# Optimization experiments

Hardware: AMD Instinct MI355X
Metric: run time of the kernel (lower is better)

## Reference

```python
import jax, jax.numpy as jnp
import numpy as np

N, E, IN, TD, H, C0, C1 = 50000, 800000, 128, 64, 4, 64, 16
SLOPE = 0.2


def setup_inputs() -> dict:
    key = jax.random.key(0)
    ks = jax.random.split(key, 20)
    def rn(k, shape, scale=1.0):
        return jax.random.normal(k, shape, dtype=jnp.float32) * scale
    return {
        "x": rn(ks[0], (N, IN)),
        "edge_index": jax.random.randint(ks[1], (2, E), 0, N),
        "timestamps": jax.random.uniform(ks[2], (E,), dtype=jnp.float32),
        # TimeEncoder: linear(1 -> TD) then cos, then abs
        "time_w": rn(ks[3], (TD,)),
        "time_b": rn(ks[4], (TD,)),
        # GATConv layer 0: in=IN, out-per-head=C0, heads=H
        "W0": rn(ks[5], (IN, H * C0), 0.1),
        "att_src0": rn(ks[6], (H, C0), 0.1),
        "att_dst0": rn(ks[7], (H, C0), 0.1),
        "lin_edge0": rn(ks[8], (TD, H * C0), 0.1),
        "att_edge0": rn(ks[9], (H, C0), 0.1),
        "bias0": rn(ks[10], (H * C0,), 0.1),
        # GATConv layer 1: in=H*C0, out-per-head=C1, heads=H
        "W1": rn(ks[11], (H * C0, H * C1), 0.1),
        "att_src1": rn(ks[12], (H, C1), 0.1),
        "att_dst1": rn(ks[13], (H, C1), 0.1),
        "lin_edge1": rn(ks[14], (TD, H * C1), 0.1),
        "att_edge1": rn(ks[15], (H, C1), 0.1),
        "bias1": rn(ks[16], (H * C1,), 0.1),
    }


def gat_layer(h_in, src, dst, edge_attr, W, a_src, a_dst, W_e, a_e, bias):
    """One PyG-style GATConv with edge-attr attention (concat heads, no dropout)."""
    heads = a_src.shape[0]
    HC = W.shape[1]
    C = HC // heads
    n_nodes = h_in.shape[0]
    h = (h_in @ W).reshape(n_nodes, heads, C)                 # [N, H, C]
    e = (edge_attr @ W_e).reshape(-1, heads, C)               # [Et, H, C]
    # attention logits per edge, per head
    alpha = ((h * a_src).sum(-1)[src]
             + (h * a_dst).sum(-1)[dst]
             + (e * a_e).sum(-1))                              # [Et, H]
    alpha = jnp.where(alpha >= 0, alpha, SLOPE * alpha)       # leaky relu
    # segment softmax over destination node
    m = jax.ops.segment_max(alpha, dst, num_segments=n_nodes)  # [N, H]
    ea = jnp.exp(alpha - m[dst])
    s = jax.ops.segment_sum(ea, dst, num_segments=n_nodes)
    a = ea / (s[dst] + 1e-16)                                 # [Et, H]
    # weighted scatter-add aggregation
    out = jax.ops.segment_sum(h[src] * a[..., None], dst, num_segments=n_nodes)
    return out.reshape(n_nodes, HC) + bias


def reference(x, edge_index, timestamps, time_w, time_b,
              W0, att_src0, att_dst0, lin_edge0, att_edge0, bias0,
              W1, att_src1, att_dst1, lin_edge1, att_edge1, bias1):
    # TimeEncoder -> abs, per-edge feature [E, TD]
    ef = jnp.abs(jnp.cos(timestamps[:, None] * time_w + time_b))
    # add self loops with edge_attr fill value 1.0
    loops = jnp.arange(N)
    src = jnp.concatenate([edge_index[0], loops])
    dst = jnp.concatenate([edge_index[1], loops])
    ef = jnp.concatenate([ef, jnp.ones((N, TD), ef.dtype)], axis=0)
    h = gat_layer(x, src, dst, ef, W0, att_src0, att_dst0, lin_edge0, att_edge0, bias0)
    h = gat_layer(h, src, dst, ef, W1, att_src1, att_dst1, lin_edge1, att_edge1, bias1)
    return h  # [N, H*C1] = [50000, 64]
```

## Files before the change

### kernel.cpp

```cpp
#include <hip/hip_runtime.h>
#include <math.h>

#define N_NODES 50000
#define N_EDGES 800000
#define ET (N_EDGES + N_NODES)
#define IN_F 128
#define TDIM 64
#define HEADS 4
#define C0 64
#define C1 16
#define HC0 256
#define HC1 64
#define KF 512
#define SLOPE 0.2f
#define TAB 4096
#define BSHIFT 8
#define NBUCKET 196
#define CHUNK 2048

using short8 = __attribute__((ext_vector_type(8))) short;
using f32x4 = __attribute__((ext_vector_type(4))) float;

__device__ __forceinline__ float bf2f(unsigned u16) { return __uint_as_float(u16 << 16); }
__device__ __forceinline__ unsigned short f2bf(float f) {
    unsigned u = __float_as_uint(f);
    return (unsigned short)((u + 0x7fffu + ((u >> 16) & 1u)) >> 16);
}
__device__ __forceinline__ unsigned pk2(float lo, float hi) {
    return (unsigned)f2bf(lo) | ((unsigned)f2bf(hi) << 16);
}
__device__ __forceinline__ float lrelu(float a) { return a >= 0.f ? a : SLOPE * a; }

__global__ __launch_bounds__(256) void k_param(
    const float* __restrict__ le0, const float* __restrict__ at0, const float* __restrict__ le1,
    const float* __restrict__ at1, const float* __restrict__ W0, const float* __restrict__ asr,
    const float* __restrict__ ads, const float* __restrict__ W1, const float* __restrict__ bias0,
    float* __restrict__ v0, float* __restrict__ v1, float* __restrict__ l0,
    float* __restrict__ l1, float* __restrict__ as0, float* __restrict__ ad0,
    unsigned short* __restrict__ W01t, float* __restrict__ b01) {
    int b = blockIdx.x, tid = threadIdx.x;
    int h = tid >> 6, c = tid & 63;
    if (b < 64) {
        int td = b;
        float p0 = le0[td * HC0 + h * C0 + c] * at0[h * C0 + c];
        for (int m = 1; m < 64; m <<= 1) p0 += __shfl_xor(p0, m);
        if (c == 0) v0[td * 4 + h] = p0;
        float p1 = 0.f;
        if (c < C1) p1 = le1[td * HC1 + h * C1 + c] * at1[h * C1 + c];
        for (int m = 1; m < 16; m <<= 1) p1 += __shfl_xor(p1, m);
        if (c == 0) v1[td * 4 + h] = p1;
    } else if (b == 64) {
        float s0 = 0.f;
        for (int td = 0; td < TDIM; ++td) s0 += le0[td * HC0 + h * C0 + c];
        s0 *= at0[h * C0 + c];
        for (int m = 1; m < 64; m <<= 1) s0 += __shfl_xor(s0, m);
        if (c == 0) l0[h] = s0;
        float s1 = 0.f;
        if (c < C1) {
            for (int td = 0; td < TDIM; ++td) s1 += le1[td * HC1 + h * C1 + c];
            s1 *= at1[h * C1 + c];
        }
        for (int m = 1; m < 16; m <<= 1) s1 += __shfl_xor(s1, m);
        if (c == 0) l1[h] = s1;
    } else if (b < 193) {
        int k = b - 65;
        float wv = W0[k * HC0 + h * C0 + c];
        float ps = wv * asr[h * C0 + c];
        float pd = wv * ads[h * C0 + c];
        for (int m = 1; m < 64; m <<= 1) {
            ps += __shfl_xor(ps, m);
            pd += __shfl_xor(pd, m);
        }
        if (c == 0) {
            as0[h * IN_F + k] = ps;
            ad0[h * IN_F + k] = pd;
        }
    } else if (b < 321) {
        int hk = (b - 193) * 4 + (tid >> 6);
        int c1 = tid & 63;
        int hh = hk >> 7, k = hk & 127;
        float acc = 0.f;
        for (int c0 = 0; c0 < C0; ++c0)
            acc += W0[k * HC0 + hh * C0 + c0] * W1[(size_t)(hh * C0 + c0) * HC1 + c1];
        W01t[(size_t)c1 * KF + hk] = f2bf(acc);
    } else {
        if (tid < 64) {
            float acc = 0.f;
            for (int k = 0; k < HC0; ++k) acc += bias0[k] * W1[(size_t)k * HC1 + tid];
            b01[tid] = acc;
        }
    }
}

__global__ __launch_bounds__(256) void k_aetab(const float* __restrict__ tw,
                                               const float* __restrict__ tb,
                                               const float* __restrict__ v0,
                                               const float* __restrict__ v1,
                                               float* __restrict__ tab0,
                                               float* __restrict__ tab1) {
    __shared__ float sw[TDIM], sb[TDIM], sv0[TDIM * 4], sv1[TDIM * 4];
    int tid = threadIdx.x;
    if (tid < TDIM) {
        sw[tid] = tw[tid];
        sb[tid] = tb[tid];
    }
    sv0[tid] = v0[tid];
    sv1[tid] = v1[tid];
    __syncthreads();
    int i = blockIdx.x * 256 + tid;
    if (i > TAB) return;
    float time = (float)i / (float)TAB;
    float a00 = 0, a01 = 0, a02 = 0, a03 = 0, a10 = 0, a11 = 0, a12 = 0, a13 = 0;
#pragma unroll 8
    for (int d = 0; d < TDIM; ++d) {
        float f = fabsf(__cosf(time * sw[d] + sb[d]));
        a00 += f * sv0[d * 4 + 0];
        a01 += f * sv0[d * 4 + 1];
        a02 += f * sv0[d * 4 + 2];
        a03 += f * sv0[d * 4 + 3];
        a10 += f * sv1[d * 4 + 0];
        a11 += f * sv1[d * 4 + 1];
        a12 += f * sv1[d * 4 + 2];
        a13 += f * sv1[d * 4 + 3];
    }
    ((float4*)tab0)[i] = make_float4(a00, a01, a02, a03);
    ((float4*)tab1)[i] = make_float4(a10, a11, a12, a13);
}

__global__ __launch_bounds__(256) void k_xbs(const float* __restrict__ x,
                                             const float* __restrict__ as0,
                                             const float* __restrict__ ad0,
                                             unsigned short* __restrict__ xb,
                                             float* __restrict__ ssrc, float* __restrict__ sdst) {
    int w = threadIdx.x >> 6, l = threadIdx.x & 63;
    int n = blockIdx.x * 4 + w;
    if (n >= N_NODES) return;
    float2 xv = *(const float2*)(x + (size_t)n * IN_F + l * 2);
    *(unsigned*)(xb + (size_t)n * IN_F + l * 2) = pk2(xv.x, xv.y);
    float ps[4], pd[4];
#pragma unroll
    for (int h = 0; h < 4; ++h) {
        float2 a = *(const float2*)(as0 + h * IN_F + l * 2);
        float2 d = *(const float2*)(ad0 + h * IN_F + l * 2);
        ps[h] = xv.x * a.x + xv.y * a.y;
        pd[h] = xv.x * d.x + xv.y * d.y;
    }
#pragma unroll
    for (int m = 1; m < 64; m <<= 1) {
#pragma unroll
        for (int h = 0; h < 4; ++h) {
            ps[h] += __shfl_xor(ps[h], m);
            pd[h] += __shfl_xor(pd[h], m);
        }
    }
    if (l == 0) {
#pragma unroll
        for (int h = 0; h < 4; ++h) {
            ssrc[n * 4 + h] = ps[h];
            sdst[n * 4 + h] = pd[h];
        }
    }
}

__global__ void k_count(const int* __restrict__ ei, int* __restrict__ deg) {
    int t = blockIdx.x * blockDim.x + threadIdx.x;
    if (t >= N_EDGES) return;
    atomicAdd(&deg[ei[N_EDGES + t]], 1);
}

__global__ void k_scan_block(const int* __restrict__ deg, int* __restrict__ rowptr,
                             int* __restrict__ blocksum, int n) {
    __shared__ int buf[256];
    int tid = threadIdx.x, i = blockIdx.x * 256 + tid;
    int v = (i < n) ? (deg[i] + 1) : 0;
    buf[tid] = v;
    __syncthreads();
    for (int off = 1; off < 256; off <<= 1) {
        int t = (tid >= off) ? buf[tid - off] : 0;
        __syncthreads();
        buf[tid] += t;
        __syncthreads();
    }
    if (i < n) rowptr[i + 1] = buf[tid];
    if (tid == 255) blocksum[blockIdx.x] = buf[255];
}

__global__ void k_scan_top(const int* __restrict__ blocksum, int* __restrict__ blockoff, int nb) {
    __shared__ int buf[256];
    int tid = threadIdx.x;
    int v = (tid < nb) ? blocksum[tid] : 0;
    buf[tid] = v;
    __syncthreads();
    for (int off = 1; off < 256; off <<= 1) {
        int t = (tid >= off) ? buf[tid - off] : 0;
        __syncthreads();
        buf[tid] += t;
        __syncthreads();
    }
    if (tid < nb) blockoff[tid] = buf[tid] - v;
}

__global__ void k_finalize(int* __restrict__ rowptr, const int* __restrict__ blockoff,
                           const int* __restrict__ deg, int* __restrict__ cursor,
                           int* __restrict__ edst, int* __restrict__ eord,
                           int* __restrict__ bcur) {
    int i = blockIdx.x * 256 + threadIdx.x;
    if (i >= N_NODES) return;
    int v = rowptr[i + 1] + blockoff[blockIdx.x];
    rowptr[i + 1] = v;
    int start = v - deg[i] - 1;
    cursor[i] = start;
    if (i == 0) rowptr[0] = 0;
    if ((i & 255) == 0) bcur[i >> BSHIFT] = start;
    for (int p = start; p < v; ++p) edst[p] = i;
    eord[v - 1] = N_EDGES + i;
}

__global__ __launch_bounds__(256) void k_bucketA(const int* __restrict__ ei,
                                                 int* __restrict__ bcur,
                                                 int2* __restrict__ staging) {
    __shared__ int cnt[NBUCKET], base[NBUCKET];
    int tid = threadIdx.x;
    int e0 = blockIdx.x * CHUNK;
    for (int i = tid; i < NBUCKET; i += 256) cnt[i] = 0;
    __syncthreads();
    int t[8], d[8];
#pragma unroll
    for (int i = 0; i < 8; ++i) {
        int tt = e0 + i * 256 + tid;
        t[i] = tt;
        d[i] = (tt < N_EDGES) ? ei[N_EDGES + tt] : -1;
        if (d[i] >= 0) atomicAdd(&cnt[d[i] >> BSHIFT], 1);
    }
    __syncthreads();
    for (int i = tid; i < NBUCKET; i += 256) {
        int c = cnt[i];
        base[i] = c ? atomicAdd(&bcur[i], c) : 0;
        cnt[i] = 0;
    }
    __syncthreads();
#pragma unroll
    for (int i = 0; i < 8; ++i) {
        if (d[i] >= 0) {
            int b = d[i] >> BSHIFT;
            int off = atomicAdd(&cnt[b], 1);
            staging[base[b] + off] = make_int2(t[i], d[i]);
        }
    }
}

__global__ __launch_bounds__(256) void k_bucketB(const int* __restrict__ rowptr,
                                                 const int* __restrict__ bcur,
                                                 const int2* __restrict__ staging,
                                                 int* __restrict__ cursor,
                                                 int* __restrict__ eord) {
    int b = blockIdx.x;
    int lo = rowptr[b << BSHIFT];
    int hi = bcur[b];
    for (int p = lo + threadIdx.x; p < hi; p += 256) {
        int2 td = staging[p];
        int q = atomicAdd(&cursor[td.y], 1);
        eord[q] = td.x;
    }
}

__global__ void k_expand(const int* __restrict__ eord, const int* __restrict__ ei,
                         const float* __restrict__ ts, const int* __restrict__ edst,
                         const float* __restrict__ tab0, const float* __restrict__ l0,
                         const float* __restrict__ ssrc0, const float* __restrict__ sdst0,
                         int* __restrict__ esrc, float* __restrict__ ew0p) {
    int p = blockIdx.x * blockDim.x + threadIdx.x;
    if (p >= ET) return;
    int t = eord[p], d = edst[p];
    int s;
    float4 a0;
    if (t >= N_EDGES) {
        s = t - N_EDGES;
        a0 = ((const float4*)l0)[0];
    } else {
        s = ei[t];
        float f = ts[t] * (float)TAB;
        int i = (int)f;
        i = i > TAB - 1 ? TAB - 1 : i;
        float fr = f - (float)i;
        float4 t0 = ((const float4*)tab0)[i];
        float4 t1 = ((const float4*)tab0)[i + 1];
        a0.x = t0.x + fr * (t1.x - t0.x);
        a0.y = t0.y + fr * (t1.y - t0.y);
        a0.z = t0.z + fr * (t1.z - t0.z);
        a0.w = t0.w + fr * (t1.w - t0.w);
    }
    esrc[p] = s;
    float4 sv = ((const float4*)ssrc0)[s];
    float4 dv = ((const float4*)sdst0)[d];
    float4 w;
    w.x = __expf(lrelu(sv.x + dv.x + a0.x));
    w.y = __expf(lrelu(sv.y + dv.y + a0.y));
    w.z = __expf(lrelu(sv.z + dv.z + a0.z));
    w.w = __expf(lrelu(sv.w + dv.w + a0.w));
    ((float4*)ew0p)[p] = w;
}

__global__ void k_ew1(const int* __restrict__ eord, const float* __restrict__ ts,
                      const int* __restrict__ esrc, const int* __restrict__ edst,
                      const float* __restrict__ tab1, const float* __restrict__ l1,
                      const float* __restrict__ ssrc, const float* __restrict__ sdst,
                      float* __restrict__ ew1p) {
    int p = blockIdx.x * blockDim.x + threadIdx.x;
    if (p >= ET) return;
    int t = eord[p];
    float4 av;
    if (t >= N_EDGES) {
        av = ((const float4*)l1)[0];
    } else {
        float f = ts[t] * (float)TAB;
        int i = (int)f;
        i = i > TAB - 1 ? TAB - 1 : i;
        float fr = f - (float)i;
        float4 t0 = ((const float4*)tab1)[i];
        float4 t1 = ((const float4*)tab1)[i + 1];
        av.x = t0.x + fr * (t1.x - t0.x);
        av.y = t0.y + fr * (t1.y - t0.y);
        av.z = t0.z + fr * (t1.z - t0.z);
        av.w = t0.w + fr * (t1.w - t0.w);
    }
    int s = esrc[p], d = edst[p];
    float4 sv = ((const float4*)ssrc)[s];
    float4 dv = ((const float4*)sdst)[d];
    float4 w;
    w.x = __expf(lrelu(sv.x + dv.x + av.x));
    w.y = __expf(lrelu(sv.y + dv.y + av.y));
    w.z = __expf(lrelu(sv.z + dv.z + av.z));
    w.w = __expf(lrelu(sv.w + dv.w + av.w));
    ((float4*)ew1p)[p] = w;
}

__global__ __launch_bounds__(256) void k_aggx(const unsigned short* __restrict__ xb,
                                              const int* __restrict__ esrc,
                                              const float* __restrict__ ew0p,
                                              const int* __restrict__ rowptr,
                                              unsigned short* __restrict__ aggx) {
    int grp = threadIdx.x >> 4, lo = threadIdx.x & 15;
    int n = blockIdx.x * 16 + grp;
    if (n >= N_NODES) return;
    int p0 = rowptr[n], p1 = rowptr[n + 1];
    float acc[4][8];
#pragma unroll
    for (int h = 0; h < 4; ++h)
#pragma unroll
        for (int j = 0; j < 8; ++j) acc[h][j] = 0.f;
    float ss0 = 0, ss1 = 0, ss2 = 0, ss3 = 0;
    float4 e_cur = ((const float4*)ew0p)[p0];
    uint4 x_cur = *(const uint4*)(xb + (size_t)esrc[p0] * IN_F + lo * 8);
    for (int p = p0; p < p1; ++p) {
        float4 e = e_cur;
        uint4 xv = x_cur;
        if (p + 1 < p1) {
            e_cur = ((const float4*)ew0p)[p + 1];
            x_cur = *(const uint4*)(xb + (size_t)esrc[p + 1] * IN_F + lo * 8);
        }
        float f[8];
        f[0] = bf2f(xv.x & 0xffff);
        f[1] = bf2f(xv.x >> 16);
        f[2] = bf2f(xv.y & 0xffff);
        f[3] = bf2f(xv.y >> 16);
        f[4] = bf2f(xv.z & 0xffff);
        f[5] = bf2f(xv.z >> 16);
        f[6] = bf2f(xv.w & 0xffff);
        f[7] = bf2f(xv.w >> 16);
#pragma unroll
        for (int j = 0; j < 8; ++j) {
            acc[0][j] += e.x * f[j];
            acc[1][j] += e.y * f[j];
            acc[2][j] += e.z * f[j];
            acc[3][j] += e.w * f[j];
        }
        ss0 += e.x;
        ss1 += e.y;
        ss2 += e.z;
        ss3 += e.w;
    }
    float inv[4] = {1.f / (ss0 + 1e-16f), 1.f / (ss1 + 1e-16f), 1.f / (ss2 + 1e-16f),
                    1.f / (ss3 + 1e-16f)};
    size_t base = (size_t)n * KF + lo * 8;
#pragma unroll
    for (int h = 0; h < 4; ++h) {
        uint4 r;
        r.x = pk2(acc[h][0] * inv[h], acc[h][1] * inv[h]);
        r.y = pk2(acc[h][2] * inv[h], acc[h][3] * inv[h]);
        r.z = pk2(acc[h][4] * inv[h], acc[h][5] * inv[h]);
        r.w = pk2(acc[h][6] * inv[h], acc[h][7] * inv[h]);
        *(uint4*)(aggx + base + h * IN_F) = r;
    }
}

__global__ __launch_bounds__(256) void k_gemm1s(
    const unsigned short* __restrict__ A, const unsigned short* __restrict__ Bt,
    const float* __restrict__ b01, const float* __restrict__ a_src,
    const float* __restrict__ a_dst, unsigned short* __restrict__ h1b, float* __restrict__ ssrc,
    float* __restrict__ sdst) {
    __shared__ unsigned short As[128 * 40];
    __shared__ unsigned short Bs[64 * 40];
    int tid = threadIdx.x, w = tid >> 6, l = tid & 63, lo = l & 15, hi = l >> 4;
    int m0 = blockIdx.x * 128;
    f32x4 acc[2][4];
#pragma unroll
    for (int i = 0; i < 2; ++i)
#pragma unroll
        for (int j = 0; j < 4; ++j) acc[i][j] = (f32x4){0.f, 0.f, 0.f, 0.f};
    int arow4 = tid >> 2, aseg = tid & 3;
    for (int k0 = 0; k0 < KF; k0 += 32) {
#pragma unroll
        for (int hf = 0; hf < 2; ++hf) {
            int arow = hf * 64 + arow4;
            uint4 va = {0, 0, 0, 0};
            if (m0 + arow < N_NODES)
                va = *(const uint4*)(A + (size_t)(m0 + arow) * KF + k0 + aseg * 8);
            *(uint4*)&As[arow * 40 + aseg * 8] = va;
        }
        uint4 vb = *(const uint4*)(Bt + (size_t)arow4 * KF + k0 + aseg * 8);
        *(uint4*)&Bs[arow4 * 40 + aseg * 8] = vb;
        __syncthreads();
        short8 af[2], bf[4];
#pragma unroll
        for (int fa = 0; fa < 2; ++fa)
            af[fa] = *(const short8*)&As[(w * 32 + fa * 16 + lo) * 40 + hi * 8];
#pragma unroll
        for (int nf = 0; nf < 4; ++nf) bf[nf] = *(const short8*)&Bs[(nf * 16 + lo) * 40 + hi * 8];
#pragma unroll
        for (int fa = 0; fa < 2; ++fa)
#pragma unroll
            for (int nf = 0; nf < 4; ++nf)
                acc[fa][nf] =
                    __builtin_amdgcn_mfma_f32_16x16x32_bf16(af[fa], bf[nf], acc[fa][nf], 0, 0, 0);
        __syncthreads();
    }
    float asv[4], adv[4], bv[4];
#pragma unroll
    for (int nf = 0; nf < 4; ++nf) {
        asv[nf] = a_src[nf * 16 + lo];
        adv[nf] = a_dst[nf * 16 + lo];
        bv[nf] = b01[nf * 16 + lo];
    }
#pragma unroll
    for (int fa = 0; fa < 2; ++fa)
#pragma unroll
        for (int r = 0; r < 4; ++r) {
            int row = m0 + w * 32 + fa * 16 + hi * 4 + r;
#pragma unroll
            for (int nf = 0; nf < 4; ++nf) {
                float v = acc[fa][nf][r] + bv[nf];
                if (row < N_NODES) h1b[(size_t)row * HC1 + nf * 16 + lo] = f2bf(v);
                float ps = v * asv[nf], pd = v * adv[nf];
                for (int m = 1; m < 16; m <<= 1) {
                    ps += __shfl_xor(ps, m);
                    pd += __shfl_xor(pd, m);
                }
                if (lo == 0 && row < N_NODES) {
                    ssrc[row * 4 + nf] = ps;
                    sdst[row * 4 + nf] = pd;
                }
            }
        }
}

__global__ __launch_bounds__(256) void k_agg1(
    const unsigned short* __restrict__ h1b, const int* __restrict__ esrc,
    const float* __restrict__ ew1p, const int* __restrict__ rowptr,
    const float* __restrict__ bias, float* __restrict__ out) {
    int grp = threadIdx.x >> 4, lo = threadIdx.x & 15;
    int n = blockIdx.x * 16 + grp;
    if (n >= N_NODES) return;
    int head = lo >> 2;
    int p0 = rowptr[n], p1 = rowptr[n + 1];
    float a0 = 0, a1 = 0, a2 = 0, a3 = 0, ss = 0;
    float e_cur = ew1p[p0 * 4 + head];
    uint2 h_cur = *(const uint2*)(h1b + (size_t)esrc[p0] * HC1 + lo * 4);
    for (int p = p0; p < p1; ++p) {
        float e = e_cur;
        uint2 hv = h_cur;
        if (p + 1 < p1) {
            e_cur = ew1p[(p + 1) * 4 + head];
            h_cur = *(const uint2*)(h1b + (size_t)esrc[p + 1] * HC1 + lo * 4);
        }
        a0 += e * bf2f(hv.x & 0xffff);
        a1 += e * bf2f(hv.x >> 16);
        a2 += e * bf2f(hv.y & 0xffff);
        a3 += e * bf2f(hv.y >> 16);
        ss += e;
    }
    float inv = 1.f / (ss + 1e-16f);
    float4 b4 = *(const float4*)(bias + lo * 4);
    float4 r = make_float4(a0 * inv + b4.x, a1 * inv + b4.y, a2 * inv + b4.z, a3 * inv + b4.w);
    *(float4*)(out + (size_t)n * HC1 + lo * 4) = r;
}

extern "C" void kernel_launch(void* const* d_in, const int* in_sizes, int n_in, void* d_out,
                              int out_size, void* d_ws, size_t ws_size, hipStream_t stream) {
    const float* x = (const float*)d_in[0];
    const int* ei = (const int*)d_in[1];
    const float* ts = (const float*)d_in[2];
    const float* time_w = (const float*)d_in[3];
    const float* time_b = (const float*)d_in[4];
    const float* W0 = (const float*)d_in[5];
    const float* att_src0 = (const float*)d_in[6];
    const float* att_dst0 = (const float*)d_in[7];
    const float* lin_edge0 = (const float*)d_in[8];
    const float* att_edge0 = (const float*)d_in[9];
    const float* bias0 = (const float*)d_in[10];
    const float* W1 = (const float*)d_in[11];
    const float* att_src1 = (const float*)d_in[12];
    const float* att_dst1 = (const float*)d_in[13];
    const float* lin_edge1 = (const float*)d_in[14];
    const float* att_edge1 = (const float*)d_in[15];
    const float* bias1 = (const float*)d_in[16];
    float* out = (float*)d_out;

    char* ws = (char*)d_ws;
    size_t off = 0;
    auto alloc = [&](size_t bytes) -> void* {
        void* p = ws + off;
        off = (off + bytes + 255) & ~(size_t)255;
        return p;
    };
    unsigned short* xb = (unsigned short*)alloc((size_t)N_NODES * IN_F * 2);
    unsigned short* aggx = (unsigned short*)alloc((size_t)N_NODES * KF * 2);
    unsigned short* h1b = (unsigned short*)alloc((size_t)N_NODES * HC1 * 2);
    unsigned short* W01t = (unsigned short*)alloc((size_t)HC1 * KF * 2);
    float* b01 = (float*)alloc(HC1 * 4);
    float* as0 = (float*)alloc(4 * IN_F * 4);
    float* ad0 = (float*)alloc(4 * IN_F * 4);
    float* tab0 = (float*)alloc((size_t)(TAB + 1) * 4 * 4);
    float* tab1 = (float*)alloc((size_t)(TAB + 1) * 4 * 4);
    float* ew0p = (float*)alloc((size_t)ET * 4 * 4);
    float* ew1p = (float*)alloc((size_t)ET * 4 * 4);
    float* ssrc0 = (float*)alloc((size_t)N_NODES * 4 * 4);
    float* sdst0 = (float*)alloc((size_t)N_NODES * 4 * 4);
    float* ssrc1 = (float*)alloc((size_t)N_NODES * 4 * 4);
    float* sdst1 = (float*)alloc((size_t)N_NODES * 4 * 4);
    float* v0 = (float*)alloc(TDIM * 4 * 4);
    float* v1 = (float*)alloc(TDIM * 4 * 4);
    float* l0 = (float*)alloc(16);
    float* l1 = (float*)alloc(16);
    int* deg = (int*)alloc((size_t)N_NODES * 4);
    int* rowptr = (int*)alloc((size_t)(N_NODES + 1) * 4);
    int* cursor = (int*)alloc((size_t)(N_NODES + 1) * 4);
    int* blocksum = (int*)alloc(256 * 4);
    int* blockoff = (int*)alloc(256 * 4);
    int* bcur = (int*)alloc(NBUCKET * 4);
    int2* staging = (int2*)alloc((size_t)ET * 8);
    int* eord = (int*)alloc((size_t)ET * 4);
    int* esrc = (int*)alloc((size_t)ET * 4);
    int* edst = (int*)alloc((size_t)ET * 4);
    (void)ws_size;
    (void)in_sizes;
    (void)n_in;
    (void)out_size;

    int nb = (N_NODES + 255) / 256;
    int ebks = (ET + 255) / 256;
    int rbks = (N_EDGES + 255) / 256;
    int cbks = (N_EDGES + CHUNK - 1) / CHUNK;
    int gx = (N_NODES + 127) / 128;
    int nblk16 = (N_NODES + 15) / 16;
    int nblk4 = (N_NODES + 3) / 4;

    k_param<<<322, 256, 0, stream>>>(lin_edge0, att_edge0, lin_edge1, att_edge1, W0, att_src0,
                                     att_dst0, W1, bias0, v0, v1, l0, l1, as0, ad0, W01t, b01);
    k_aetab<<<(TAB + 256) / 256, 256, 0, stream>>>(time_w, time_b, v0, v1, tab0, tab1);

    k_xbs<<<nblk4, 256, 0, stream>>>(x, as0, ad0, xb, ssrc0, sdst0);

    hipMemsetAsync(deg, 0, (size_t)N_NODES * 4, stream);
    k_count<<<rbks, 256, 0, stream>>>(ei, deg);
    k_scan_block<<<nb, 256, 0, stream>>>(deg, rowptr, blocksum, N_NODES);
    k_scan_top<<<1, 256, 0, stream>>>(blocksum, blockoff, nb);
    k_finalize<<<nb, 256, 0, stream>>>(rowptr, blockoff, deg, cursor, edst, eord, bcur);
    k_bucketA<<<cbks, 256, 0, stream>>>(ei, bcur, staging);
    k_bucketB<<<NBUCKET, 256, 0, stream>>>(rowptr, bcur, staging, cursor, eord);

    k_expand<<<ebks, 256, 0, stream>>>(eord, ei, ts, edst, tab0, l0, ssrc0, sdst0, esrc, ew0p);

    k_aggx<<<nblk16, 256, 0, stream>>>(xb, esrc, ew0p, rowptr, aggx);

    k_gemm1s<<<gx, 256, 0, stream>>>(aggx, W01t, b01, att_src1, att_dst1, h1b, ssrc1, sdst1);
    k_ew1<<<ebks, 256, 0, stream>>>(eord, ts, esrc, edst, tab1, l1, ssrc1, sdst1, ew1p);
    k_agg1<<<nblk16, 256, 0, stream>>>(h1b, esrc, ew1p, rowptr, bias1, out);
}
```

Measured before the change: 269.2 us.

## Carry src and timestamp through bucketing, fuse layer-1 edge weights into aggregation

The bucket sort now stages (src, dst, timestamp) so the CSR pass writes esrc and a permuted timestamp array directly. This removes the eord indirection and the gather of ei and ts in k_expand. The separate k_ew1 kernel and its ew1p buffer are dropped; k_agg1 computes the layer-1 attention exponent inline per edge and head. Both aggregation kernels become grid-stride loops over a fixed 1024 blocks, and k_aggx prefetches esrc two edges ahead. In exchange the staging entries grow from 8 to 16 bytes, and self-loops are now marked by a negative timestamp sentinel.

New measurement: 298.3 us. 10.8% more time.

```diff
diff --git a/kernel.cpp b/kernel.cpp
--- a/kernel.cpp
+++ b/kernel.cpp
@@ -17,6 +17,8 @@
 #define BSHIFT 8
 #define NBUCKET 196
 #define CHUNK 2048
+#define AGG_BLOCKS 1024
+#define NGRP (AGG_BLOCKS * 16)
 
 using short8 = __attribute__((ext_vector_type(8))) short;
 using f32x4 = __attribute__((ext_vector_type(4))) float;
@@ -202,8 +204,8 @@
 
 __global__ void k_finalize(int* __restrict__ rowptr, const int* __restrict__ blockoff,
                            const int* __restrict__ deg, int* __restrict__ cursor,
-                           int* __restrict__ edst, int* __restrict__ eord,
-                           int* __restrict__ bcur) {
+                           int* __restrict__ edst, int* __restrict__ esrc,
+                           float* __restrict__ tsp, int* __restrict__ bcur) {
     int i = blockIdx.x * 256 + threadIdx.x;
     if (i >= N_NODES) return;
     int v = rowptr[i + 1] + blockoff[blockIdx.x];
@@ -213,24 +215,31 @@
     if (i == 0) rowptr[0] = 0;
     if ((i & 255) == 0) bcur[i >> BSHIFT] = start;
     for (int p = start; p < v; ++p) edst[p] = i;
-    eord[v - 1] = N_EDGES + i;
+    esrc[v - 1] = i;
+    tsp[v - 1] = -1.f;
 }
 
 __global__ __launch_bounds__(256) void k_bucketA(const int* __restrict__ ei,
+                                                 const float* __restrict__ ts,
                                                  int* __restrict__ bcur,
-                                                 int2* __restrict__ staging) {
+                                                 int4* __restrict__ staging) {
     __shared__ int cnt[NBUCKET], base[NBUCKET];
     int tid = threadIdx.x;
     int e0 = blockIdx.x * CHUNK;
     for (int i = tid; i < NBUCKET; i += 256) cnt[i] = 0;
     __syncthreads();
-    int t[8], d[8];
+    int s[8], d[8], tv[8];
 #pragma unroll
     for (int i = 0; i < 8; ++i) {
         int tt = e0 + i * 256 + tid;
-        t[i] = tt;
-        d[i] = (tt < N_EDGES) ? ei[N_EDGES + tt] : -1;
-        if (d[i] >= 0) atomicAdd(&cnt[d[i] >> BSHIFT], 1);
+        if (tt < N_EDGES) {
+            s[i] = ei[tt];
+            d[i] = ei[N_EDGES + tt];
+            tv[i] = __float_as_int(ts[tt]);
+            atomicAdd(&cnt[d[i] >> BSHIFT], 1);
+        } else {
+            d[i] = -1;
+        }
     }
     __syncthreads();
     for (int i = tid; i < NBUCKET; i += 256) {
@@ -244,42 +253,40 @@
         if (d[i] >= 0) {
             int b = d[i] >> BSHIFT;
             int off = atomicAdd(&cnt[b], 1);
-            staging[base[b] + off] = make_int2(t[i], d[i]);
+            staging[base[b] + off] = make_int4(s[i], d[i], tv[i], 0);
         }
     }
 }
 
 __global__ __launch_bounds__(256) void k_bucketB(const int* __restrict__ rowptr,
                                                  const int* __restrict__ bcur,
-                                                 const int2* __restrict__ staging,
+                                                 const int4* __restrict__ staging,
                                                  int* __restrict__ cursor,
-                                                 int* __restrict__ eord) {
+                                                 int* __restrict__ esrc,
+                                                 float* __restrict__ tsp) {
     int b = blockIdx.x;
     int lo = rowptr[b << BSHIFT];
     int hi = bcur[b];
     for (int p = lo + threadIdx.x; p < hi; p += 256) {
-        int2 td = staging[p];
-        int q = atomicAdd(&cursor[td.y], 1);
-        eord[q] = td.x;
-    }
-}
-
-__global__ void k_expand(const int* __restrict__ eord, const int* __restrict__ ei,
-                         const float* __restrict__ ts, const int* __restrict__ edst,
-                         const float* __restrict__ tab0, const float* __restrict__ l0,
-                         const float* __restrict__ ssrc0, const float* __restrict__ sdst0,
-                         int* __restrict__ esrc, float* __restrict__ ew0p) {
+        int4 sdt = staging[p];
+        int q = atomicAdd(&cursor[sdt.y], 1);
+        esrc[q] = sdt.x;
+        tsp[q] = __int_as_float(sdt.z);
+    }
+}
+
+__global__ void k_expand(const int* __restrict__ esrc, const int* __restrict__ edst,
+                         const float* __restrict__ tsp, const float* __restrict__ tab0,
+                         const float* __restrict__ l0, const float* __restrict__ ssrc0,
+                         const float* __restrict__ sdst0, float* __restrict__ ew0p) {
     int p = blockIdx.x * blockDim.x + threadIdx.x;
     if (p >= ET) return;
-    int t = eord[p], d = edst[p];
-    int s;
+    float tv = tsp[p];
     float4 a0;
-    if (t >= N_EDGES) {
-        s = t - N_EDGES;
+    if (tv < 0.f) {
         a0 = ((const float4*)l0)[0];
     } else {
-        s = ei[t];
-        float f = ts[t] * (float)TAB;
+        float f = tv * (float)TAB;
         int i = (int)f;
         i = i > TAB - 1 ? TAB - 1 : i;
         float fr = f - (float)i;
@@ -290,7 +297,7 @@
         a0.z = t0.z + fr * (t1.z - t0.z);
         a0.w = t0.w + fr * (t1.w - t0.w);
     }
-    esrc[p] = s;
+    int s = esrc[p], d = edst[p];
     float4 sv = ((const float4*)ssrc0)[s];
     float4 dv = ((const float4*)sdst0)[d];
     float4 w;
@@ -301,96 +308,65 @@
     ((float4*)ew0p)[p] = w;
 }
 
-__global__ void k_ew1(const int* __restrict__ eord, const float* __restrict__ ts,
-                      const int* __restrict__ esrc, const int* __restrict__ edst,
-                      const float* __restrict__ tab1, const float* __restrict__ l1,
-                      const float* __restrict__ ssrc, const float* __restrict__ sdst,
-                      float* __restrict__ ew1p) {
-    int p = blockIdx.x * blockDim.x + threadIdx.x;
-    if (p >= ET) return;
-    int t = eord[p];
-    float4 av;
-    if (t >= N_EDGES) {
-        av = ((const float4*)l1)[0];
-    } else {
-        float f = ts[t] * (float)TAB;
-        int i = (int)f;
-        i = i > TAB - 1 ? TAB - 1 : i;
-        float fr = f - (float)i;
-        float4 t0 = ((const float4*)tab1)[i];
-        float4 t1 = ((const float4*)tab1)[i + 1];
-        av.x = t0.x + fr * (t1.x - t0.x);
-        av.y = t0.y + fr * (t1.y - t0.y);
-        av.z = t0.z + fr * (t1.z - t0.z);
-        av.w = t0.w + fr * (t1.w - t0.w);
-    }
-    int s = esrc[p], d = edst[p];
-    float4 sv = ((const float4*)ssrc)[s];
-    float4 dv = ((const float4*)sdst)[d];
-    float4 w;
-    w.x = __expf(lrelu(sv.x + dv.x + av.x));
-    w.y = __expf(lrelu(sv.y + dv.y + av.y));
-    w.z = __expf(lrelu(sv.z + dv.z + av.z));
-    w.w = __expf(lrelu(sv.w + dv.w + av.w));
-    ((float4*)ew1p)[p] = w;
-}
-
 __global__ __launch_bounds__(256) void k_aggx(const unsigned short* __restrict__ xb,
                                               const int* __restrict__ esrc,
                                               const float* __restrict__ ew0p,
                                               const int* __restrict__ rowptr,
                                               unsigned short* __restrict__ aggx) {
-    int grp = threadIdx.x >> 4, lo = threadIdx.x & 15;
-    int n = blockIdx.x * 16 + grp;
-    if (n >= N_NODES) return;
-    int p0 = rowptr[n], p1 = rowptr[n + 1];
-    float acc[4][8];
-#pragma unroll
-    for (int h = 0; h < 4; ++h)
-#pragma unroll
-        for (int j = 0; j < 8; ++j) acc[h][j] = 0.f;
-    float ss0 = 0, ss1 = 0, ss2 = 0, ss3 = 0;
-    float4 e_cur = ((const float4*)ew0p)[p0];
-    uint4 x_cur = *(const uint4*)(xb + (size_t)esrc[p0] * IN_F + lo * 8);
-    for (int p = p0; p < p1; ++p) {
-        float4 e = e_cur;
-        uint4 xv = x_cur;
-        if (p + 1 < p1) {
-            e_cur = ((const float4*)ew0p)[p + 1];
-            x_cur = *(const uint4*)(xb + (size_t)esrc[p + 1] * IN_F + lo * 8);
-        }
-        float f[8];
-        f[0] = bf2f(xv.x & 0xffff);
-        f[1] = bf2f(xv.x >> 16);
-        f[2] = bf2f(xv.y & 0xffff);
-        f[3] = bf2f(xv.y >> 16);
-        f[4] = bf2f(xv.z & 0xffff);
-        f[5] = bf2f(xv.z >> 16);
-        f[6] = bf2f(xv.w & 0xffff);
-        f[7] = bf2f(xv.w >> 16);
-#pragma unroll
-        for (int j = 0; j < 8; ++j) {
-            acc[0][j] += e.x * f[j];
-            acc[1][j] += e.y * f[j];
-            acc[2][j] += e.z * f[j];
-            acc[3][j] += e.w * f[j];
-        }
-        ss0 += e.x;
-        ss1 += e.y;
-        ss2 += e.z;
-        ss3 += e.w;
-    }
-    float inv[4] = {1.f / (ss0 + 1e-16f), 1.f / (ss1 + 1e-16f), 1.f / (ss2 + 1e-16f),
-                    1.f / (ss3 + 1e-16f)};
-    size_t base = (size_t)n * KF + lo * 8;
-#pragma unroll
-    for (int h = 0; h < 4; ++h) {
-        uint4 r;
-        r.x = pk2(acc[h][0] * inv[h], acc[h][1] * inv[h]);
-        r.y = pk2(acc[h][2] * inv[h], acc[h][3] * inv[h]);
-        r.z = pk2(acc[h][4] * inv[h], acc[h][5] * inv[h]);
-        r.w = pk2(acc[h][6] * inv[h], acc[h][7] * inv[h]);
-        *(uint4*)(aggx + base + h * IN_F) = r;
+    int g0 = blockIdx.x * 16 + (threadIdx.x >> 4);
+    int lo = threadIdx.x & 15;
+    for (int n = g0; n < N_NODES; n += NGRP) {
+        int p0 = rowptr[n], p1 = rowptr[n + 1];
+        float acc[4][8];
+#pragma unroll
+        for (int h = 0; h < 4; ++h)
+#pragma unroll
+            for (int j = 0; j < 8; ++j) acc[h][j] = 0.f;
+        float ss0 = 0, ss1 = 0, ss2 = 0, ss3 = 0;
+        float4 e_cur = ((const float4*)ew0p)[p0];
+        uint4 x_cur = *(const uint4*)(xb + (size_t)esrc[p0] * IN_F + lo * 8);
+        int s_nxt = (p0 + 1 < p1) ? esrc[p0 + 1] : 0;
+        for (int p = p0; p < p1; ++p) {
+            float4 e = e_cur;
+            uint4 xv = x_cur;
+            if (p + 1 < p1) {
+                e_cur = ((const float4*)ew0p)[p + 1];
+                x_cur = *(const uint4*)(xb + (size_t)s_nxt * IN_F + lo * 8);
+                if (p + 2 < p1) s_nxt = esrc[p + 2];
+            }
+            float f[8];
+            f[0] = bf2f(xv.x & 0xffff);
+            f[1] = bf2f(xv.x >> 16);
+            f[2] = bf2f(xv.y & 0xffff);
+            f[3] = bf2f(xv.y >> 16);
+            f[4] = bf2f(xv.z & 0xffff);
+            f[5] = bf2f(xv.z >> 16);
+            f[6] = bf2f(xv.w & 0xffff);
+            f[7] = bf2f(xv.w >> 16);
+#pragma unroll
+            for (int j = 0; j < 8; ++j) {
+                acc[0][j] += e.x * f[j];
+                acc[1][j] += e.y * f[j];
+                acc[2][j] += e.z * f[j];
+                acc[3][j] += e.w * f[j];
+            }
+            ss0 += e.x;
+            ss1 += e.y;
+            ss2 += e.z;
+            ss3 += e.w;
+        }
+        float inv[4] = {1.f / (ss0 + 1e-16f), 1.f / (ss1 + 1e-16f), 1.f / (ss2 + 1e-16f),
+                        1.f / (ss3 + 1e-16f)};
+        size_t base = (size_t)n * KF + lo * 8;
+#pragma unroll
+        for (int h = 0; h < 4; ++h) {
+            uint4 r;
+            r.x = pk2(acc[h][0] * inv[h], acc[h][1] * inv[h]);
+            r.y = pk2(acc[h][2] * inv[h], acc[h][3] * inv[h]);
+            r.z = pk2(acc[h][4] * inv[h], acc[h][5] * inv[h]);
+            r.w = pk2(acc[h][6] * inv[h], acc[h][7] * inv[h]);
+            *(uint4*)(aggx + base + h * IN_F) = r;
+        }
     }
 }
 
@@ -466,33 +442,55 @@
 
 __global__ __launch_bounds__(256) void k_agg1(
     const unsigned short* __restrict__ h1b, const int* __restrict__ esrc,
-    const float* __restrict__ ew1p, const int* __restrict__ rowptr,
+    const float* __restrict__ tsp, const float* __restrict__ tab1,
+    const float* __restrict__ l1, const float* __restrict__ ssrc,
+    const float* __restrict__ sdst, const int* __restrict__ rowptr,
     const float* __restrict__ bias, float* __restrict__ out) {
-    int grp = threadIdx.x >> 4, lo = threadIdx.x & 15;
-    int n = blockIdx.x * 16 + grp;
-    if (n >= N_NODES) return;
+    int g0 = blockIdx.x * 16 + (threadIdx.x >> 4);
+    int lo = threadIdx.x & 15;
     int head = lo >> 2;
-    int p0 = rowptr[n], p1 = rowptr[n + 1];
-    float a0 = 0, a1 = 0, a2 = 0, a3 = 0, ss = 0;
-    float e_cur = ew1p[p0 * 4 + head];
-    uint2 h_cur = *(const uint2*)(h1b + (size_t)esrc[p0] * HC1 + lo * 4);
-    for (int p = p0; p < p1; ++p) {
-        float e = e_cur;
-        uint2 hv = h_cur;
-        if (p + 1 < p1) {
-            e_cur = ew1p[(p + 1) * 4 + head];
-            h_cur = *(const uint2*)(h1b + (size_t)esrc[p + 1] * HC1 + lo * 4);
-        }
-        a0 += e * bf2f(hv.x & 0xffff);
-        a1 += e * bf2f(hv.x >> 16);
-        a2 += e * bf2f(hv.y & 0xffff);
-        a3 += e * bf2f(hv.y >> 16);
-        ss += e;
-    }
-    float inv = 1.f / (ss + 1e-16f);
-    float4 b4 = *(const float4*)(bias + lo * 4);
-    float4 r = make_float4(a0 * inv + b4.x, a1 * inv + b4.y, a2 * inv + b4.z, a3 * inv + b4.w);
-    *(float4*)(out + (size_t)n * HC1 + lo * 4) = r;
+    float lav = l1[head];
+    for (int n = g0; n < N_NODES; n += NGRP) {
+        float sdv = sdst[n * 4 + head];
+        int p0 = rowptr[n], p1 = rowptr[n + 1];
+        float a0 = 0, a1 = 0, a2 = 0, a3 = 0, ss = 0;
+        int s_cur = esrc[p0];
+        float t_cur = tsp[p0];
+        uint2 h_cur = *(const uint2*)(h1b + (size_t)s_cur * HC1 + lo * 4);
+        for (int p = p0; p < p1; ++p) {
+            int s = s_cur;
+            float tv = t_cur;
+            uint2 hv = h_cur;
+            if (p + 1 < p1) {
+                s_cur = esrc[p + 1];
+                t_cur = tsp[p + 1];
+                h_cur = *(const uint2*)(h1b + (size_t)s_cur * HC1 + lo * 4);
+            }
+            float av;
+            if (tv < 0.f) {
+                av = lav;
+            } else {
+                float f = tv * (float)TAB;
+                int i = (int)f;
+                i = i > TAB - 1 ? TAB - 1 : i;
+                float fr = f - (float)i;
+                float t0 = tab1[i * 4 + head];
+                float t1 = tab1[(i + 1) * 4 + head];
+                av = t0 + fr * (t1 - t0);
+            }
+            float e = __expf(lrelu(ssrc[s * 4 + head] + sdv + av));
+            a0 += e * bf2f(hv.x & 0xffff);
+            a1 += e * bf2f(hv.x >> 16);
+            a2 += e * bf2f(hv.y & 0xffff);
+            a3 += e * bf2f(hv.y >> 16);
+            ss += e;
+        }
+        float inv = 1.f / (ss + 1e-16f);
+        float4 b4 = *(const float4*)(bias + lo * 4);
+        float4 r =
+            make_float4(a0 * inv + b4.x, a1 * inv + b4.y, a2 * inv + b4.z, a3 * inv + b4.w);
+        *(float4*)(out + (size_t)n * HC1 + lo * 4) = r;
+    }
 }
 
 extern "C" void kernel_launch(void* const* d_in, const int* in_sizes, int n_in, void* d_out,
@@ -533,7 +531,6 @@
     float* tab0 = (float*)alloc((size_t)(TAB + 1) * 4 * 4);
     float* tab1 = (float*)alloc((size_t)(TAB + 1) * 4 * 4);
     float* ew0p = (float*)alloc((size_t)ET * 4 * 4);
-    float* ew1p = (float*)alloc((size_t)ET * 4 * 4);
     float* ssrc0 = (float*)alloc((size_t)N_NODES * 4 * 4);
     float* sdst0 = (float*)alloc((size_t)N_NODES * 4 * 4);
     float* ssrc1 = (float*)alloc((size_t)N_NODES * 4 * 4);
@@ -542,14 +539,14 @@
     float* v1 = (float*)alloc(TDIM * 4 * 4);
     float* l0 = (float*)alloc(16);
     float* l1 = (float*)alloc(16);
+    float* tsp = (float*)alloc((size_t)ET * 4);
     int* deg = (int*)alloc((size_t)N_NODES * 4);
     int* rowptr = (int*)alloc((size_t)(N_NODES + 1) * 4);
     int* cursor = (int*)alloc((size_t)(N_NODES + 1) * 4);
     int* blocksum = (int*)alloc(256 * 4);
     int* blockoff = (int*)alloc(256 * 4);
     int* bcur = (int*)alloc(NBUCKET * 4);
-    int2* staging = (int2*)alloc((size_t)ET * 8);
-    int* eord = (int*)alloc((size_t)ET * 4);
+    int4* staging = (int4*)alloc((size_t)ET * 16);
     int* esrc = (int*)alloc((size_t)ET * 4);
     int* edst = (int*)alloc((size_t)ET * 4);
     (void)ws_size;
@@ -562,7 +559,6 @@
     int rbks = (N_EDGES + 255) / 256;
     int cbks = (N_EDGES + CHUNK - 1) / CHUNK;
     int gx = (N_NODES + 127) / 128;
-    int nblk16 = (N_NODES + 15) / 16;
     int nblk4 = (N_NODES + 3) / 4;
 
     k_param<<<322, 256, 0, stream>>>(lin_edge0, att_edge0, lin_edge1, att_edge1, W0, att_src0,
@@ -575,15 +571,15 @@
     k_count<<<rbks, 256, 0, stream>>>(ei, deg);
     k_scan_block<<<nb, 256, 0, stream>>>(deg, rowptr, blocksum, N_NODES);
     k_scan_top<<<1, 256, 0, stream>>>(blocksum, blockoff, nb);
-    k_finalize<<<nb, 256, 0, stream>>>(rowptr, blockoff, deg, cursor, edst, eord, bcur);
-    k_bucketA<<<cbks, 256, 0, stream>>>(ei, bcur, staging);
-    k_bucketB<<<NBUCKET, 256, 0, stream>>>(rowptr, bcur, staging, cursor, eord);
-
-    k_expand<<<ebks, 256, 0, stream>>>(eord, ei, ts, edst, tab0, l0, ssrc0, sdst0, esrc, ew0p);
-
-    k_aggx<<<nblk16, 256, 0, stream>>>(xb, esrc, ew0p, rowptr, aggx);
+    k_finalize<<<nb, 256, 0, stream>>>(rowptr, blockoff, deg, cursor, edst, esrc, tsp, bcur);
+    k_bucketA<<<cbks, 256, 0, stream>>>(ei, ts, bcur, staging);
+    k_bucketB<<<NBUCKET, 256, 0, stream>>>(rowptr, bcur, staging, cursor, esrc, tsp);
+
+    k_expand<<<ebks, 256, 0, stream>>>(esrc, edst, tsp, tab0, l0, ssrc0, sdst0, ew0p);
+
+    k_aggx<<<AGG_BLOCKS, 256, 0, stream>>>(xb, esrc, ew0p, rowptr, aggx);
 
     k_gemm1s<<<gx, 256, 0, stream>>>(aggx, W01t, b01, att_src1, att_dst1, h1b, ssrc1, sdst1);
-    k_ew1<<<ebks, 256, 0, stream>>>(eord, ts, esrc, edst, tab1, l1, ssrc1, sdst1, ew1p);
-    k_agg1<<<nblk16, 256, 0, stream>>>(h1b, esrc, ew1p, rowptr, bias1, out);
-}
+    k_agg1<<<AGG_BLOCKS, 256, 0, stream>>>(h1b, esrc, tsp, tab1, l1, ssrc1, sdst1, rowptr, bias1,
+                                           out);
+}
```
